# Performance work log

Measured on AMD Instinct MI355X. Metric: run time of the kernel, lower is better.

The kernel has to match this reference:

```python
import jax, jax.numpy as jnp
import numpy as np

MOMENTUM = 0.999
TEMP = 0.07
NUM_HARD_NEGS = 16
NUM_CLASSES = 20000


def _normalize(x, axis=-1, eps=1e-12):
    n = jnp.linalg.norm(x, axis=axis, keepdims=True)
    return x / jnp.maximum(n, eps)


def setup_inputs() -> dict:
    key = jax.random.key(0)
    k1, k2, k3, k4, k5 = jax.random.split(key, 5)
    B, K, Dp, De, C = 512, 8, 256, 512, NUM_CLASSES
    return {
        "part_features": jax.random.normal(k1, (B, K, Dp), dtype=jnp.float32),
        "embeddings": jax.random.normal(k2, (B, De), dtype=jnp.float32),
        "sat_emb": jax.random.normal(k3, (B, De), dtype=jnp.float32),
        "part_bank": jax.random.normal(k4, (C, K, Dp), dtype=jnp.float32) * 0.01,
        "embed_bank": jax.random.normal(k5, (C, De), dtype=jnp.float32) * 0.01,
        "labels": jnp.arange(B, dtype=jnp.int64),
    }


def reference(part_features, embeddings, sat_emb, part_bank, embed_bank, labels):
    m = MOMENTUM
    B = embeddings.shape[0]
    C = embed_bank.shape[0]

    # --- EMA scatter update (bank assumed initialized for all classes) ---
    # labels are distinct, so vectorized scatter == sequential python loop.
    new_part_bank = part_bank.at[labels].set(
        m * part_bank[labels] + (1.0 - m) * part_features)
    new_embed_bank = embed_bank.at[labels].set(
        m * embed_bank[labels] + (1.0 - m) * embeddings)

    # Banks are torch buffers updated under no_grad -> stop_gradient.
    eb = jax.lax.stop_gradient(new_embed_bank)

    # --- PrototypeNCE ---
    q = _normalize(embeddings)                      # [B, De]
    protos = _normalize(eb)                         # [C, De]
    sim = (q @ protos.T) / TEMP                     # [B, C]
    pos_sim = jnp.take_along_axis(sim, labels[:, None], axis=1)  # [B, 1]
    class_ids = jnp.arange(C)
    pos_mask = labels[:, None] == class_ids[None, :]
    neg_sim = jnp.where(pos_mask, -1e9, sim)
    hard_negs, _ = jax.lax.top_k(neg_sim, NUM_HARD_NEGS)          # [B, k]
    logits = jnp.concatenate([pos_sim, hard_negs], axis=1)       # [B, 1+k]
    nce_loss = jnp.mean(jax.nn.logsumexp(logits, axis=1) - logits[:, 0])

    # --- Cross-view prototype alignment ---
    p = _normalize(eb[labels])                      # [B, De]
    d = _normalize(embeddings)
    s = _normalize(sat_emb)
    align_loss = 0.5 * (jnp.mean(1.0 - jnp.sum(d * p, axis=-1))
                        + jnp.mean(1.0 - jnp.sum(s * p, axis=-1)))

    return new_part_bank, new_embed_bank, nce_loss, align_loss
```

## Files before the change

### kernel.cpp

```cpp
#include <hip/hip_runtime.h>
#include <math.h>

#define MOM 0.999f
#define ONE_M_MOM 0.001f
#define INV_TEMP (1.0f / 0.07f)
#define C_CLASSES 20000
#define B_SZ 512
#define DE 512
#define PART_ROW 2048
#define PART_BANK_N (C_CLASSES * PART_ROW)
#define EMB_BANK_N (C_CLASSES * DE)
#define NEG_INF (-3.0e38f)
#define NTILE 157
#define NT2 (NTILE * 2)
#define NGEMM (4 * NTILE)

typedef __attribute__((ext_vector_type(8))) short short8;
typedef __attribute__((ext_vector_type(4))) float f32x4;

__device__ inline unsigned short f2bf_rne(float f) {
    unsigned u = __builtin_bit_cast(unsigned, f);
    return (unsigned short)((u + 0x7FFFu + ((u >> 16) & 1u)) >> 16);
}

__device__ inline float bf2f(unsigned short u) {
    return __builtin_bit_cast(float, (unsigned)u << 16);
}

__device__ inline void gload16(const void* g, void* l) {
    __builtin_amdgcn_global_load_lds(
        (const __attribute__((address_space(1))) unsigned int*)g,
        (__attribute__((address_space(3))) unsigned int*)l, 16, 0, 0);
}

__global__ void build_map(const int* __restrict__ labels, int* __restrict__ inv_map) {
    __shared__ int lab[B_SZ];
    int t = threadIdx.x;
    lab[t] = labels[t];
    lab[t + 256] = labels[t + 256];
    __syncthreads();
    int c = blockIdx.x * 256 + t;
    if (c >= C_CLASSES) return;
    int m = -1;
    for (int i = 0; i < B_SZ; ++i)
        if (lab[i] == c) m = i;
    inv_map[c] = m;
}

__global__ void embed_qnorm(const float* __restrict__ ebank, const float* __restrict__ emb,
                            const int* __restrict__ inv_map, float* __restrict__ out_eb,
                            unsigned short* __restrict__ Bb, float* __restrict__ inv_norm,
                            float* __restrict__ q_hat, unsigned short* __restrict__ Ab) {
    int w = threadIdx.x >> 6, l = threadIdx.x & 63;
    int blk = blockIdx.x;
    if (blk < 5000) {
        int c = blk * 4 + w;
        const float4* row = (const float4*)(ebank + ((long)c << 9));
        float4 v0 = row[2 * l], v1 = row[2 * l + 1];
        int mb = inv_map[c];
        if (mb >= 0) {
            const float4* nr = (const float4*)(emb + ((long)mb << 9));
            float4 n0 = nr[2 * l], n1 = nr[2 * l + 1];
            v0.x = MOM * v0.x + ONE_M_MOM * n0.x;
            v0.y = MOM * v0.y + ONE_M_MOM * n0.y;
            v0.z = MOM * v0.z + ONE_M_MOM * n0.z;
            v0.w = MOM * v0.w + ONE_M_MOM * n0.w;
            v1.x = MOM * v1.x + ONE_M_MOM * n1.x;
            v1.y = MOM * v1.y + ONE_M_MOM * n1.y;
            v1.z = MOM * v1.z + ONE_M_MOM * n1.z;
            v1.w = MOM * v1.w + ONE_M_MOM * n1.w;
        }
        float4* orow = (float4*)(out_eb + ((long)c << 9));
        orow[2 * l] = v0; orow[2 * l + 1] = v1;
        float ss = v0.x * v0.x + v0.y * v0.y + v0.z * v0.z + v0.w * v0.w
                 + v1.x * v1.x + v1.y * v1.y + v1.z * v1.z + v1.w * v1.w;
#pragma unroll
        for (int off = 32; off; off >>= 1) ss += __shfl_xor(ss, off);
        if (l == 0) inv_norm[c] = 1.0f / fmaxf(sqrtf(ss), 1e-12f);
        short8 o;
        o[0] = (short)f2bf_rne(v0.x); o[1] = (short)f2bf_rne(v0.y);
        o[2] = (short)f2bf_rne(v0.z); o[3] = (short)f2bf_rne(v0.w);
        o[4] = (short)f2bf_rne(v1.x); o[5] = (short)f2bf_rne(v1.y);
        o[6] = (short)f2bf_rne(v1.z); o[7] = (short)f2bf_rne(v1.w);
        *(short8*)(Bb + ((long)c << 9) + l * 8) = o;
    } else {
        int b = (blk - 5000) * 4 + w;
        const float4* row = (const float4*)(emb + ((long)b << 9));
        float4 v0 = row[2 * l], v1 = row[2 * l + 1];
        float ss = v0.x * v0.x + v0.y * v0.y + v0.z * v0.z + v0.w * v0.w
                 + v1.x * v1.x + v1.y * v1.y + v1.z * v1.z + v1.w * v1.w;
#pragma unroll
        for (int off = 32; off; off >>= 1) ss += __shfl_xor(ss, off);
        float inv = 1.0f / fmaxf(sqrtf(ss), 1e-12f);
        v0.x *= inv; v0.y *= inv; v0.z *= inv; v0.w *= inv;
        v1.x *= inv; v1.y *= inv; v1.z *= inv; v1.w *= inv;
        float4* outq = (float4*)(q_hat + ((long)b << 9));
        outq[2 * l] = v0; outq[2 * l + 1] = v1;
        short8 o;
        o[0] = (short)f2bf_rne(v0.x); o[1] = (short)f2bf_rne(v0.y);
        o[2] = (short)f2bf_rne(v0.z); o[3] = (short)f2bf_rne(v0.w);
        o[4] = (short)f2bf_rne(v1.x); o[5] = (short)f2bf_rne(v1.y);
        o[6] = (short)f2bf_rne(v1.z); o[7] = (short)f2bf_rne(v1.w);
        *(short8*)(Ab + ((long)b << 9) + l * 8) = o;
    }
}

__global__ void __launch_bounds__(256)
part_gemm(const unsigned short* __restrict__ A, const unsigned short* __restrict__ B,
          const float* __restrict__ inv_norm, const int* __restrict__ labels,
          float* __restrict__ partials,
          const float4* __restrict__ pb, const float4* __restrict__ pf,
          const int* __restrict__ inv_map, float4* __restrict__ out_pb) {
    if (blockIdx.x >= NGEMM) {
        int c = blockIdx.x - NGEMM;
        int t = threadIdx.x;
        long base = (long)c * (PART_ROW / 4);
        int mb = inv_map[c];
        if (mb >= 0) {
            const float4* src = pf + (long)mb * (PART_ROW / 4);
#pragma unroll
            for (int it = 0; it < 2; ++it) {
                int j = t + it * 256;
                float4 o = pb[base + j], n = src[j], r;
                r.x = MOM * o.x + ONE_M_MOM * n.x;
                r.y = MOM * o.y + ONE_M_MOM * n.y;
                r.z = MOM * o.z + ONE_M_MOM * n.z;
                r.w = MOM * o.w + ONE_M_MOM * n.w;
                out_pb[base + j] = r;
            }
        } else {
#pragma unroll
            for (int it = 0; it < 2; ++it) {
                int j = t + it * 256;
                out_pb[base + j] = pb[base + j];
            }
        }
        return;
    }

    __shared__ unsigned short smem[128 * 130];
    unsigned short* Asm = smem;
    unsigned short* Bsm = smem + 8192;

    const int t = threadIdx.x;
    const int w = t >> 6, l = t & 63;
    const int wr = w >> 1, wc = w & 1;

    int id = blockIdx.x;
    int xcd = id & 7, idx = id >> 3;
    int wg = (xcd < 4) ? xcd * 79 + idx : 316 + (xcd - 4) * 78 + idx;
    const int bm = wg & 3, bn = wg >> 2;

    f32x4 acc[4][4] = {};

    const int srow = t >> 3;
    const long swz = ((t & 7) ^ (srow & 7)) << 3;
    const unsigned short* Ag = A + ((long)(bm * 128 + srow) << 9) + swz;
    const unsigned short* Bg[4];
#pragma unroll
    for (int i = 0; i < 4; ++i) {
        int br = bn * 128 + i * 32 + srow;
        if (br > C_CLASSES - 1) br = C_CLASSES - 1;
        Bg[i] = B + ((long)br << 9) + swz;
    }
    char* Adst = (char*)Asm + (w << 10);
    char* Bdst = (char*)Bsm + (w << 10);

    const int fr = l & 15;
    const int s4 = l >> 4;
    const int swr0 = ((s4) ^ (fr & 7)) << 4;
    const int swr1 = ((4 + s4) ^ (fr & 7)) << 4;

    for (int kt = 0; kt < 8; ++kt) {
        const int ko = kt << 6;
#pragma unroll
        for (int i = 0; i < 4; ++i) {
            gload16(Ag + ko + ((long)i << 14), Adst + (i << 12));
            gload16(Bg[i] + ko, Bdst + (i << 12));
        }
        __syncthreads();
        short8 af[2][4], bf[2][4];
        const char* Abase = (const char*)Asm;
        const char* Bbase = (const char*)Bsm;
#pragma unroll
        for (int m = 0; m < 4; ++m) {
            int ra = (wr * 64 + m * 16 + fr) << 7;
            int rb = (wc * 64 + m * 16 + fr) << 7;
            af[0][m] = *(const short8*)(Abase + ra + swr0);
            af[1][m] = *(const short8*)(Abase + ra + swr1);
            bf[0][m] = *(const short8*)(Bbase + rb + swr0);
            bf[1][m] = *(const short8*)(Bbase + rb + swr1);
        }
#pragma unroll
        for (int kk = 0; kk < 2; ++kk)
#pragma unroll
            for (int m = 0; m < 4; ++m)
#pragma unroll
                for (int n = 0; n < 4; ++n)
                    acc[m][n] = __builtin_amdgcn_mfma_f32_16x16x32_bf16(
                        af[kk][m], bf[kk][n], acc[m][n], 0, 0, 0);
        __syncthreads();
    }

    unsigned short* stile = smem;
    const int r4 = s4 << 2;
#pragma unroll
    for (int n = 0; n < 4; ++n) {
        int ct = wc * 64 + fr + n * 16;
        int cg = bn * 128 + ct;
        bool ok = cg < C_CLASSES;
        float sc = ok ? inv_norm[cg] * INV_TEMP : 0.0f;
#pragma unroll
        for (int m = 0; m < 4; ++m) {
            int rt = wr * 64 + r4 + m * 16;
#pragma unroll
            for (int j = 0; j < 4; ++j) {
                float v = ok ? acc[m][n][j] * sc : NEG_INF;
                stile[(rt + j) * 130 + ct] = f2bf_rne(v);
            }
        }
    }
    __syncthreads();

    const int r = t >> 1, half = t & 1;
    const int gr = bm * 128 + r;
    const int lab = labels[gr];
    const int lab_l = lab - (bn << 7) - (half << 6);
    const unsigned short* bp = stile + r * 130 + half * 64;
    float tl[16];
#pragma unroll
    for (int j = 0; j < 16; ++j) tl[j] = NEG_INF;
    for (int c = 0; c < 64; ++c) {
        if (c == lab_l) continue;
        float v = bf2f(bp[c]);
        if (v > tl[15]) {
            tl[15] = v;
#pragma unroll
            for (int j = 15; j > 0; --j) {
                float a = tl[j - 1], bb = tl[j];
                if (bb > a) { tl[j - 1] = bb; tl[j] = a; }
            }
        }
    }
    float* op = partials + ((long)gr * NT2 + (bn << 1) + half) * 16;
#pragma unroll
    for (int j = 0; j < 16; ++j) op[j] = tl[j];
}

__global__ void merge_nce_align(const float* __restrict__ partials,
                                const float* __restrict__ q_hat,
                                const float* __restrict__ out_eb,
                                const float* __restrict__ sat,
                                const float* __restrict__ inv_norm,
                                const int* __restrict__ labels,
                                float* __restrict__ lnce, float* __restrict__ lalign) {
    int b = blockIdx.x;
    int l = threadIdx.x;
    const float* pr = partials + (long)b * (NT2 * 16);

    float tl[16];
#pragma unroll
    for (int j = 0; j < 16; ++j) tl[j] = NEG_INF;
    for (int i = l; i < NT2 * 16; i += 64) {
        float v = pr[i];
        if (v > tl[15]) {
            tl[15] = v;
#pragma unroll
            for (int j = 15; j > 0; --j) {
                float a = tl[j - 1], bb = tl[j];
                if (bb > a) { tl[j - 1] = bb; tl[j] = a; }
            }
        }
    }

    float M = 0.f, S = 0.f;
#pragma unroll 1
    for (int j = 0; j < 16; ++j) {
        float v = tl[0];
        float mx = v;
#pragma unroll
        for (int off = 32; off; off >>= 1) mx = fmaxf(mx, __shfl_xor(mx, off));
        unsigned long long ball = __ballot(v == mx);
        int win = (int)(__ffsll((unsigned long long)ball)) - 1;
        if (l == win) {
#pragma unroll
            for (int q = 0; q < 15; ++q) tl[q] = tl[q + 1];
            tl[15] = NEG_INF;
        }
        if (j == 0) { M = mx; S = 1.0f; }
        else S += expf(mx - M);
    }

    int lab = labels[b];
    const float4* qr = (const float4*)(q_hat + ((long)b << 9));
    const float4* er = (const float4*)(out_eb + ((long)lab << 9));
    const float4* sr = (const float4*)(sat + ((long)b << 9));
    float a1 = 0.f, a2 = 0.f, a3 = 0.f;
#pragma unroll
    for (int rr = 0; rr < 2; ++rr) {
        int j = 2 * l + rr;
        float4 d4 = qr[j], s4 = sr[j], e4 = er[j];
        a1 += d4.x * e4.x + d4.y * e4.y + d4.z * e4.z + d4.w * e4.w;
        a2 += s4.x * e4.x + s4.y * e4.y + s4.z * e4.z + s4.w * e4.w;
        a3 += s4.x * s4.x + s4.y * s4.y + s4.z * s4.z + s4.w * s4.w;
    }
#pragma unroll
    for (int off = 32; off; off >>= 1) {
        a1 += __shfl_xor(a1, off);
        a2 += __shfl_xor(a2, off);
        a3 += __shfl_xor(a3, off);
    }
    if (l == 0) {
        float invl = inv_norm[lab];
        float pos = a1 * invl * INV_TEMP;
        float mx2 = fmaxf(M, pos);
        float ssum = expf(M - mx2) * S + expf(pos - mx2);
        lnce[b] = logf(ssum) + mx2 - pos;
        float pd = a1 * invl;
        float ps = a2 * invl / fmaxf(sqrtf(a3), 1e-12f);
        lalign[b] = 1.0f - 0.5f * (pd + ps);
    }
}

__global__ void finalize(const float* __restrict__ lnce, const float* __restrict__ lalign,
                         float* __restrict__ out_losses) {
    __shared__ float s1[256], s2[256];
    int t = threadIdx.x;
    s1[t] = lnce[t] + lnce[t + 256];
    s2[t] = lalign[t] + lalign[t + 256];
    __syncthreads();
    for (int s = 128; s; s >>= 1) {
        if (t < s) { s1[t] += s1[t + s]; s2[t] += s2[t + s]; }
        __syncthreads();
    }
    if (t == 0) {
        out_losses[0] = s1[0] / (float)B_SZ;
        out_losses[1] = s2[0] / (float)B_SZ;
    }
}

extern "C" void kernel_launch(void* const* d_in, const int* in_sizes, int n_in,
                              void* d_out, int out_size, void* d_ws, size_t ws_size,
                              hipStream_t stream) {
    const float* pf = (const float*)d_in[0];
    const float* emb = (const float*)d_in[1];
    const float* sat = (const float*)d_in[2];
    const float* pb = (const float*)d_in[3];
    const float* ebank = (const float*)d_in[4];
    const int* labels = (const int*)d_in[5];

    float* out = (float*)d_out;
    float* out_pb = out;
    float* out_eb = out + PART_BANK_N;
    float* out_losses = out + PART_BANK_N + EMB_BANK_N;

    float* ws = (float*)d_ws;
    float* q_hat = ws;
    float* inv_norm = q_hat + (long)B_SZ * DE;
    int* inv_map = (int*)(inv_norm + C_CLASSES);
    float* lnce = (float*)(inv_map + C_CLASSES);
    float* lalign = lnce + B_SZ;
    float* partials = lalign + B_SZ;
    unsigned short* Ab = (unsigned short*)(partials + (long)B_SZ * NT2 * 16);
    unsigned short* Bb = Ab + (long)B_SZ * DE;

    build_map<<<(C_CLASSES + 255) / 256, 256, 0, stream>>>(labels, inv_map);
    embed_qnorm<<<5000 + 128, 256, 0, stream>>>(ebank, emb, inv_map, out_eb, Bb, inv_norm,
                                                q_hat, Ab);
    part_gemm<<<NGEMM + C_CLASSES, 256, 0, stream>>>(Ab, Bb, inv_norm, labels, partials,
                                                     (const float4*)pb, (const float4*)pf,
                                                     inv_map, (float4*)out_pb);
    merge_nce_align<<<B_SZ, 64, 0, stream>>>(partials, q_hat, out_eb, sat, inv_norm,
                                             labels, lnce, lalign);
    finalize<<<1, 256, 0, stream>>>(lnce, lalign, out_losses);
}
```

Before: 160.0 us.

## Drop label-map and finalize kernels; batch part-bank copy eight classes per block

Removes the build_map kernel: each wave now finds its class's batch index by scanning the labels with a wave-wide max reduction, and part-bank blocks build a small shared-memory map for their classes. Each part-bank block now handles eight classes with sixteen float4 loads in flight per thread, cutting the block count from 20000 to 2500. The finalize kernel is folded into the merge kernel through an atomic counter, so the last block computes the mean losses. This saves two launches and raises memory-level parallelism in the copy, at the cost of redundant label scans in every wave and a dependence on the counter being reset correctly.

```diff
diff --git a/kernel.cpp b/kernel.cpp
--- a/kernel.cpp
+++ b/kernel.cpp
@@ -14,6 +14,7 @@
 #define NTILE 157
 #define NT2 (NTILE * 2)
 #define NGEMM (4 * NTILE)
+#define NPART 2500
 
 typedef __attribute__((ext_vector_type(8))) short short8;
 typedef __attribute__((ext_vector_type(4))) float f32x4;
@@ -33,33 +34,27 @@
         (__attribute__((address_space(3))) unsigned int*)l, 16, 0, 0);
 }
 
-__global__ void build_map(const int* __restrict__ labels, int* __restrict__ inv_map) {
-    __shared__ int lab[B_SZ];
-    int t = threadIdx.x;
-    lab[t] = labels[t];
-    lab[t + 256] = labels[t + 256];
-    __syncthreads();
-    int c = blockIdx.x * 256 + t;
-    if (c >= C_CLASSES) return;
-    int m = -1;
-    for (int i = 0; i < B_SZ; ++i)
-        if (lab[i] == c) m = i;
-    inv_map[c] = m;
-}
-
 __global__ void embed_qnorm(const float* __restrict__ ebank, const float* __restrict__ emb,
-                            const int* __restrict__ inv_map, float* __restrict__ out_eb,
+                            const int* __restrict__ labels, float* __restrict__ out_eb,
                             unsigned short* __restrict__ Bb, float* __restrict__ inv_norm,
-                            float* __restrict__ q_hat, unsigned short* __restrict__ Ab) {
+                            float* __restrict__ q_hat, unsigned short* __restrict__ Ab,
+                            int* __restrict__ counter) {
     int w = threadIdx.x >> 6, l = threadIdx.x & 63;
     int blk = blockIdx.x;
+    if (blk == 0 && threadIdx.x == 0) *counter = 0;
     if (blk < 5000) {
         int c = blk * 4 + w;
+        int m = -1;
+#pragma unroll
+        for (int k = 0; k < 8; ++k)
+            if (labels[l + k * 64] == c) m = l + k * 64;
+#pragma unroll
+        for (int off = 32; off; off >>= 1) m = max(m, __shfl_xor(m, off));
+
         const float4* row = (const float4*)(ebank + ((long)c << 9));
         float4 v0 = row[2 * l], v1 = row[2 * l + 1];
-        int mb = inv_map[c];
-        if (mb >= 0) {
-            const float4* nr = (const float4*)(emb + ((long)mb << 9));
+        if (m >= 0) {
+            const float4* nr = (const float4*)(emb + ((long)m << 9));
             float4 n0 = nr[2 * l], n1 = nr[2 * l + 1];
             v0.x = MOM * v0.x + ONE_M_MOM * n0.x;
             v0.y = MOM * v0.y + ONE_M_MOM * n0.y;
@@ -110,35 +105,42 @@
           const float* __restrict__ inv_norm, const int* __restrict__ labels,
           float* __restrict__ partials,
           const float4* __restrict__ pb, const float4* __restrict__ pf,
-          const int* __restrict__ inv_map, float4* __restrict__ out_pb) {
+          float4* __restrict__ out_pb) {
+    __shared__ unsigned short smem[128 * 130];
+
     if (blockIdx.x >= NGEMM) {
-        int c = blockIdx.x - NGEMM;
+        int c0 = (blockIdx.x - NGEMM) * 8;
         int t = threadIdx.x;
-        long base = (long)c * (PART_ROW / 4);
-        int mb = inv_map[c];
-        if (mb >= 0) {
-            const float4* src = pf + (long)mb * (PART_ROW / 4);
-#pragma unroll
-            for (int it = 0; it < 2; ++it) {
-                int j = t + it * 256;
-                float4 o = pb[base + j], n = src[j], r;
-                r.x = MOM * o.x + ONE_M_MOM * n.x;
-                r.y = MOM * o.y + ONE_M_MOM * n.y;
-                r.z = MOM * o.z + ONE_M_MOM * n.z;
-                r.w = MOM * o.w + ONE_M_MOM * n.w;
-                out_pb[base + j] = r;
+        int* mbs = (int*)smem;
+        if (t < 8) mbs[t] = -1;
+        __syncthreads();
+        int la = labels[t], lb = labels[t + 256];
+#pragma unroll
+        for (int r = 0; r < 8; ++r) {
+            if (la == c0 + r) mbs[r] = t;
+            if (lb == c0 + r) mbs[r] = t + 256;
+        }
+        __syncthreads();
+        const float4* src = pb + (long)c0 * (PART_ROW / 4);
+        float4* dst = out_pb + (long)c0 * (PART_ROW / 4);
+        float4 v[16];
+#pragma unroll
+        for (int i = 0; i < 16; ++i) v[i] = src[t + i * 256];
+#pragma unroll
+        for (int i = 0; i < 16; ++i) {
+            int mb = mbs[i >> 1];
+            if (mb >= 0) {
+                float4 n = pf[(long)mb * (PART_ROW / 4) + (t + (i & 1) * 256)];
+                v[i].x = MOM * v[i].x + ONE_M_MOM * n.x;
+                v[i].y = MOM * v[i].y + ONE_M_MOM * n.y;
+                v[i].z = MOM * v[i].z + ONE_M_MOM * n.z;
+                v[i].w = MOM * v[i].w + ONE_M_MOM * n.w;
             }
-        } else {
-#pragma unroll
-            for (int it = 0; it < 2; ++it) {
-                int j = t + it * 256;
-                out_pb[base + j] = pb[base + j];
-            }
+            dst[t + i * 256] = v[i];
         }
         return;
     }
 
-    __shared__ unsigned short smem[128 * 130];
     unsigned short* Asm = smem;
     unsigned short* Bsm = smem + 8192;
 
@@ -247,28 +249,32 @@
     for (int j = 0; j < 16; ++j) op[j] = tl[j];
 }
 
-__global__ void merge_nce_align(const float* __restrict__ partials,
-                                const float* __restrict__ q_hat,
-                                const float* __restrict__ out_eb,
-                                const float* __restrict__ sat,
-                                const float* __restrict__ inv_norm,
-                                const int* __restrict__ labels,
-                                float* __restrict__ lnce, float* __restrict__ lalign) {
+__global__ void __launch_bounds__(64)
+merge_fin(const float* __restrict__ partials, const float* __restrict__ q_hat,
+          const float* __restrict__ out_eb, const float* __restrict__ sat,
+          const float* __restrict__ inv_norm, const int* __restrict__ labels,
+          float* __restrict__ lnce, float* __restrict__ lalign,
+          int* __restrict__ counter, float* __restrict__ out_losses) {
     int b = blockIdx.x;
     int l = threadIdx.x;
-    const float* pr = partials + (long)b * (NT2 * 16);
+    const float4* pr4 = (const float4*)(partials + (long)b * (NT2 * 16));
 
     float tl[16];
 #pragma unroll
     for (int j = 0; j < 16; ++j) tl[j] = NEG_INF;
-    for (int i = l; i < NT2 * 16; i += 64) {
-        float v = pr[i];
-        if (v > tl[15]) {
-            tl[15] = v;
-#pragma unroll
-            for (int j = 15; j > 0; --j) {
-                float a = tl[j - 1], bb = tl[j];
-                if (bb > a) { tl[j - 1] = bb; tl[j] = a; }
+    for (int i = l; i < NT2 * 4; i += 64) {
+        float4 v4 = pr4[i];
+        float vv[4] = {v4.x, v4.y, v4.z, v4.w};
+#pragma unroll
+        for (int q = 0; q < 4; ++q) {
+            float v = vv[q];
+            if (v > tl[15]) {
+                tl[15] = v;
+#pragma unroll
+                for (int j = 15; j > 0; --j) {
+                    float a = tl[j - 1], bb = tl[j];
+                    if (bb > a) { tl[j - 1] = bb; tl[j] = a; }
+                }
             }
         }
     }
@@ -310,6 +316,7 @@
         a2 += __shfl_xor(a2, off);
         a3 += __shfl_xor(a3, off);
     }
+    int done = 0;
     if (l == 0) {
         float invl = inv_norm[lab];
         float pos = a1 * invl * INV_TEMP;
@@ -319,23 +326,30 @@
         float pd = a1 * invl;
         float ps = a2 * invl / fmaxf(sqrtf(a3), 1e-12f);
         lalign[b] = 1.0f - 0.5f * (pd + ps);
-    }
-}
-
-__global__ void finalize(const float* __restrict__ lnce, const float* __restrict__ lalign,
-                         float* __restrict__ out_losses) {
-    __shared__ float s1[256], s2[256];
-    int t = threadIdx.x;
-    s1[t] = lnce[t] + lnce[t + 256];
-    s2[t] = lalign[t] + lalign[t + 256];
-    __syncthreads();
-    for (int s = 128; s; s >>= 1) {
-        if (t < s) { s1[t] += s1[t + s]; s2[t] += s2[t + s]; }
-        __syncthreads();
-    }
-    if (t == 0) {
-        out_losses[0] = s1[0] / (float)B_SZ;
-        out_losses[1] = s2[0] / (float)B_SZ;
+        __threadfence();
+        done = (atomicAdd(counter, 1) == B_SZ - 1) ? 1 : 0;
+    }
+    done = __shfl(done, 0);
+    if (done) {
+        __threadfence();
+        volatile const float* vn = lnce;
+        volatile const float* va = lalign;
+        float s1 = 0.f, s2 = 0.f;
+#pragma unroll
+        for (int k = 0; k < B_SZ / 64; ++k) {
+            s1 += vn[l + k * 64];
+            s2 += va[l + k * 64];
+        }
+#pragma unroll
+        for (int off = 32; off; off >>= 1) {
+            s1 += __shfl_xor(s1, off);
+            s2 += __shfl_xor(s2, off);
+        }
+        if (l == 0) {
+            out_losses[0] = s1 / (float)B_SZ;
+            out_losses[1] = s2 / (float)B_SZ;
+            *counter = 0;
+        }
     }
 }
 
@@ -357,20 +371,18 @@
     float* ws = (float*)d_ws;
     float* q_hat = ws;
     float* inv_norm = q_hat + (long)B_SZ * DE;
-    int* inv_map = (int*)(inv_norm + C_CLASSES);
-    float* lnce = (float*)(inv_map + C_CLASSES);
+    int* counter = (int*)(inv_norm + C_CLASSES);
+    float* lnce = (float*)(counter + 16);
     float* lalign = lnce + B_SZ;
     float* partials = lalign + B_SZ;
     unsigned short* Ab = (unsigned short*)(partials + (long)B_SZ * NT2 * 16);
     unsigned short* Bb = Ab + (long)B_SZ * DE;
 
-    build_map<<<(C_CLASSES + 255) / 256, 256, 0, stream>>>(labels, inv_map);
-    embed_qnorm<<<5000 + 128, 256, 0, stream>>>(ebank, emb, inv_map, out_eb, Bb, inv_norm,
-                                                q_hat, Ab);
-    part_gemm<<<NGEMM + C_CLASSES, 256, 0, stream>>>(Ab, Bb, inv_norm, labels, partials,
-                                                     (const float4*)pb, (const float4*)pf,
-                                                     inv_map, (float4*)out_pb);
-    merge_nce_align<<<B_SZ, 64, 0, stream>>>(partials, q_hat, out_eb, sat, inv_norm,
-                                             labels, lnce, lalign);
-    finalize<<<1, 256, 0, stream>>>(lnce, lalign, out_losses);
-}
+    embed_qnorm<<<5000 + 128, 256, 0, stream>>>(ebank, emb, labels, out_eb, Bb, inv_norm,
+                                                q_hat, Ab, counter);
+    part_gemm<<<NGEMM + NPART, 256, 0, stream>>>(Ab, Bb, inv_norm, labels, partials,
+                                                 (const float4*)pb, (const float4*)pf,
+                                                 (float4*)out_pb);
+    merge_fin<<<B_SZ, 64, 0, stream>>>(partials, q_hat, out_eb, sat, inv_norm,
+                                       labels, lnce, lalign, counter, out_losses);
+}
```

After: 146.3 us. 8.6% less time.
